# Optimization experiments

Measured on AMD Instinct MI355X. Metric: run time of the kernel, lower is better.

## Reference

```python
import jax, jax.numpy as jnp
import numpy as np

P = 50          # num_predicates
E = 2000        # num_entities
M = 64          # max_facts_per_query
F = 2_000_000   # num facts
N = 500_000     # num queries
BASE = E + 2    # pack base = max(constant_no, padding_idx) + 2


def setup_inputs() -> dict:
    key = jax.random.key(0)
    k1, k2, k3, k4, k5, k6 = jax.random.split(key, 6)
    fp = jax.random.randint(k1, (F,), 0, P, dtype=jnp.int32)
    fs = jax.random.randint(k2, (F,), 0, E, dtype=jnp.int32)
    fo = jax.random.randint(k3, (F,), 0, E, dtype=jnp.int32)
    facts_idx = jnp.stack([fp, fs, fo], axis=1)  # [F, 3]
    preds = jax.random.randint(k4, (N,), 0, P, dtype=jnp.int32)
    bound_args = jax.random.randint(k5, (N,), 0, E, dtype=jnp.int32)
    direction = jax.random.randint(k6, (N,), 0, 2, dtype=jnp.int32)
    return {"facts_idx": facts_idx, "preds": preds,
            "bound_args": bound_args, "direction": direction}


def _build_csr(keys, vals, num_buckets):
    """Sort vals by key; build offset table via scatter-add + cumsum (as in torch)."""
    order = jnp.argsort(keys)               # stable sort, matches pre-hash-sorted facts
    sorted_vals = vals[order]
    counts = jnp.zeros(num_buckets + 1, dtype=jnp.int32).at[keys + 1].add(1)
    offsets = jnp.cumsum(counts)
    return sorted_vals, offsets


def reference(facts_idx, preds, bound_args, direction):
    # --- _FactIndexBase: sort facts by packed 64-bit hash (lexicographic p,s,o) ---
    fp, fs, fo = facts_idx[:, 0], facts_idx[:, 1], facts_idx[:, 2]
    hashes = (fp * BASE + fs) * BASE + fo   # fits int32 for these dims
    h_order = jnp.argsort(hashes)
    fp, fs, fo = fp[h_order], fs[h_order], fo[h_order]

    # --- _build_inverted_indices: (pred,subj)->objs and (pred,obj)->subjs CSR ---
    ps_sorted_objs, ps_offsets = _build_csr(fp * E + fs, fo, P * E)
    po_sorted_subjs, po_offsets = _build_csr(fp * E + fo, fs, P * E)

    # --- enumerate() ---
    keys = preds * E + bound_args                               # [N]
    starts_ps = ps_offsets[keys]
    counts_ps = jnp.clip(ps_offsets[keys + 1] - starts_ps, 0, M)
    starts_po = po_offsets[keys]
    counts_po = jnp.clip(po_offsets[keys + 1] - starts_po, 0, M)
    is_obj = direction == 0                                     # [N] bool
    starts = jnp.where(is_obj, starts_ps, starts_po)
    counts = jnp.where(is_obj, counts_ps, counts_po)

    pos = jnp.arange(M, dtype=jnp.int32)[None, :]               # [1, M]
    valid = pos < counts[:, None]                               # [N, M]
    size = ps_sorted_objs.shape[0]                              # == F for both arrays
    gi = jnp.clip(starts[:, None] + pos, 0, size - 1)           # [N, M]
    vals_obj = ps_sorted_objs[gi]
    vals_subj = po_sorted_subjs[gi]
    candidates = jnp.where(is_obj[:, None], vals_obj, vals_subj)
    return candidates, valid
```

## Files before the change

### kernel.cpp

```cpp
#include <hip/hip_runtime.h>

#define PCONST 50
#define ECONST 2000
#define MCONST 64
#define NKEY   (PCONST * ECONST)
#define KPB    256
#define NBIN   ((NKEY + KPB - 1) / KPB)
#define NBIN2  (2 * NBIN)
#define SC_THREADS 1024
#define SC_CHUNK   8192
#define FPT    (SC_CHUNK / SC_THREADS)
#define CAP    6144

typedef int ivec4 __attribute__((ext_vector_type(4)));

__global__ void __launch_bounds__(SC_THREADS)
scatter_sort(const int* __restrict__ facts,
             int* __restrict__ bincur,
             unsigned* __restrict__ slab, int F) {
    __shared__ unsigned ordered[2 * SC_CHUNK];
    __shared__ int cnt[NBIN2];
    __shared__ int lbase[NBIN2];
    __shared__ int cur[NBIN2];
    __shared__ int base[NBIN2];
    __shared__ int wsum[16];

    int t = threadIdx.x;
    int blockStart = blockIdx.x * SC_CHUNK;
    int n = min(SC_CHUNK, F - blockStart);
    if (n <= 0) return;

    for (int i = t; i < NBIN2; i += SC_THREADS) cnt[i] = 0;
    __syncthreads();

    int myBase = blockStart + t * FPT;
    int myN = F - myBase;
    myN = (myN < 0) ? 0 : ((myN > FPT) ? FPT : myN);

    unsigned vps[FPT], vpo[FPT];

    if (myN == FPT) {
        const int4* p = (const int4*)(facts + 3 * myBase);
        int4 w0 = p[0], w1 = p[1], w2 = p[2], w3 = p[3], w4 = p[4], w5 = p[5];
        int kps, kpo;
        kps = w0.x * ECONST + w0.y; kpo = w0.x * ECONST + w0.z;
        vps[0] = ((unsigned)kps << 11) | (unsigned)w0.z;
        vpo[0] = ((unsigned)kpo << 11) | (unsigned)w0.y;
        atomicAdd(&cnt[kps >> 8], 1); atomicAdd(&cnt[NBIN + (kpo >> 8)], 1);
        kps = w0.w * ECONST + w1.x; kpo = w0.w * ECONST + w1.y;
        vps[1] = ((unsigned)kps << 11) | (unsigned)w1.y;
        vpo[1] = ((unsigned)kpo << 11) | (unsigned)w1.x;
        atomicAdd(&cnt[kps >> 8], 1); atomicAdd(&cnt[NBIN + (kpo >> 8)], 1);
        kps = w1.z * ECONST + w1.w; kpo = w1.z * ECONST + w2.x;
        vps[2] = ((unsigned)kps << 11) | (unsigned)w2.x;
        vpo[2] = ((unsigned)kpo << 11) | (unsigned)w1.w;
        atomicAdd(&cnt[kps >> 8], 1); atomicAdd(&cnt[NBIN + (kpo >> 8)], 1);
        kps = w2.y * ECONST + w2.z; kpo = w2.y * ECONST + w2.w;
        vps[3] = ((unsigned)kps << 11) | (unsigned)w2.w;
        vpo[3] = ((unsigned)kpo << 11) | (unsigned)w2.z;
        atomicAdd(&cnt[kps >> 8], 1); atomicAdd(&cnt[NBIN + (kpo >> 8)], 1);
        kps = w3.x * ECONST + w3.y; kpo = w3.x * ECONST + w3.z;
        vps[4] = ((unsigned)kps << 11) | (unsigned)w3.z;
        vpo[4] = ((unsigned)kpo << 11) | (unsigned)w3.y;
        atomicAdd(&cnt[kps >> 8], 1); atomicAdd(&cnt[NBIN + (kpo >> 8)], 1);
        kps = w3.w * ECONST + w4.x; kpo = w3.w * ECONST + w4.y;
        vps[5] = ((unsigned)kps << 11) | (unsigned)w4.y;
        vpo[5] = ((unsigned)kpo << 11) | (unsigned)w4.x;
        atomicAdd(&cnt[kps >> 8], 1); atomicAdd(&cnt[NBIN + (kpo >> 8)], 1);
        kps = w4.z * ECONST + w4.w; kpo = w4.z * ECONST + w5.x;
        vps[6] = ((unsigned)kps << 11) | (unsigned)w5.x;
        vpo[6] = ((unsigned)kpo << 11) | (unsigned)w4.w;
        atomicAdd(&cnt[kps >> 8], 1); atomicAdd(&cnt[NBIN + (kpo >> 8)], 1);
        kps = w5.y * ECONST + w5.z; kpo = w5.y * ECONST + w5.w;
        vps[7] = ((unsigned)kps << 11) | (unsigned)w5.w;
        vpo[7] = ((unsigned)kpo << 11) | (unsigned)w5.z;
        atomicAdd(&cnt[kps >> 8], 1); atomicAdd(&cnt[NBIN + (kpo >> 8)], 1);
    } else {
        for (int i = 0; i < myN; ++i) {
            int g = myBase + i;
            int fp = facts[3 * g], fs = facts[3 * g + 1], fo = facts[3 * g + 2];
            int kps = fp * ECONST + fs;
            int kpo = fp * ECONST + fo;
            vps[i] = ((unsigned)kps << 11) | (unsigned)fo;
            vpo[i] = ((unsigned)kpo << 11) | (unsigned)fs;
            atomicAdd(&cnt[kps >> 8], 1);
            atomicAdd(&cnt[NBIN + (kpo >> 8)], 1);
        }
    }
    __syncthreads();

    {
        int lane = t & 63, w = t >> 6;
        int c = (t < NBIN2) ? cnt[t] : 0;
        int inc = c;
        for (int d = 1; d < 64; d <<= 1) {
            int v = __shfl_up(inc, d);
            if (lane >= d) inc += v;
        }
        if (lane == 63) wsum[w] = inc;
        __syncthreads();
        if (t < NBIN2) {
            int wbase = 0;
            for (int i = 0; i < w; ++i) wbase += wsum[i];
            int excl = wbase + inc - c;
            lbase[t] = excl;
            cur[t]   = excl;
        }
    }
    __syncthreads();
    for (int i = t; i < NBIN2; i += SC_THREADS) {
        int c = cnt[i];
        base[i] = c ? atomicAdd(&bincur[i], c) : 0;
    }
    __syncthreads();

    #pragma unroll
    for (int i = 0; i < FPT; ++i) {
        if (i >= myN) break;
        unsigned ps = vps[i];
        int pos = atomicAdd(&cur[ps >> 19], 1);
        ordered[pos] = ps;
        unsigned po = vpo[i];
        pos = atomicAdd(&cur[NBIN + (po >> 19)], 1);
        ordered[pos] = (1u << 28) | po;
    }
    __syncthreads();

    int n2 = 2 * n;
    for (int j = t; j < n2; j += SC_THREADS) {
        unsigned v = ordered[j];
        int cbin = (int)((v >> 19) & 511u) + ((v >> 28) ? NBIN : 0);
        int pos  = base[cbin] + (j - lbase[cbin]);
        if (pos < CAP) slab[(size_t)cbin * CAP + pos] = v & 0x0FFFFFFFu;
    }
}

__global__ void binsort_kernel(const int* __restrict__ bincur,
                               const unsigned* __restrict__ slab,
                               unsigned* __restrict__ qtab,
                               unsigned short* __restrict__ dataA,
                               int F) {
    __shared__ unsigned short outv[CAP];
    __shared__ unsigned char  keyof[CAP];
    __shared__ int hist[KPB];
    __shared__ int sbase[KPB];
    __shared__ int wsum[4];
    __shared__ int red[4];

    int wg = blockIdx.x;
    int csr = (wg < NBIN) ? 0 : 1;
    int b   = wg - csr * NBIN;
    const int* curbase = bincur + csr * NBIN;
    int gofs = csr ? (F + 64) : 0;
    int t = threadIdx.x;
    int lane = t & 63, w = t >> 6;

    int s = 0;
    for (int i = t; i < b; i += KPB) s += curbase[i];
    for (int d = 1; d < 64; d <<= 1) s += __shfl_xor(s, d);
    if (lane == 0) red[w] = s;
    __syncthreads();
    int start = red[0] + red[1] + red[2] + red[3];

    int key0 = b * KPB;
    int len  = min(curbase[b], CAP);
    const unsigned* src = slab + (size_t)wg * CAP;

    hist[t] = 0;
    __syncthreads();

    for (int i = t; i < len; i += KPB)
        atomicAdd(&hist[(int)(src[i] >> 11) - key0], 1);
    __syncthreads();

    int c = hist[t];
    int inc = c;
    for (int d = 1; d < 64; d <<= 1) {
        int v = __shfl_up(inc, d);
        if (lane >= d) inc += v;
    }
    if (lane == 63) wsum[w] = inc;
    __syncthreads();
    int wbase = 0;
    for (int i = 0; i < w; ++i) wbase += wsum[i];
    int excl = wbase + inc - c;
    int gk = key0 + t;
    if (gk < NKEY)
        qtab[csr * NKEY + gk] =
            ((unsigned)(gofs + start + excl) << 7) | (unsigned)min(c, MCONST);
    sbase[t] = excl;
    hist[t]  = excl;
    __syncthreads();

    for (int i = t; i < len; i += KPB) {
        unsigned v = src[i];
        int lk  = (int)(v >> 11) - key0;
        int pos = atomicAdd(&hist[lk], 1);
        outv[pos]  = (unsigned short)(v & 2047u);
        keyof[pos] = (unsigned char)lk;
    }
    __syncthreads();

    for (int pos = t; pos < len; pos += KPB) {
        unsigned short v = outv[pos];
        int lk = (int)keyof[pos];
        int s0 = sbase[lk];
        int e0 = hist[lk];
        int rank = 0;
        for (int j = s0; j < e0; ++j) {
            unsigned short wv = outv[j];
            rank += (wv < v) || (wv == v && j < pos);
        }
        int gpos = start + s0 + rank;
        dataA[gofs + gpos] = v;
        if (gpos == F - 1) {
            for (int j = 0; j < 64; ++j) dataA[gofs + F + j] = v;
        }
    }
}

__global__ void query_kernel(const int* __restrict__ preds,
                             const int* __restrict__ bound,
                             const int* __restrict__ dir,
                             const unsigned* __restrict__ qtab,
                             const unsigned short* __restrict__ dataA,
                             int* __restrict__ cand,
                             int* __restrict__ valid, int N) {
    int gwave  = (blockIdx.x * blockDim.x + threadIdx.x) >> 6;
    int lane   = threadIdx.x & 63;
    int nwaves = (gridDim.x * blockDim.x) >> 6;
    int grp = lane >> 4;
    int sl  = (lane & 15) * 4;

    for (int qb = gwave * 64; qb < N; qb += nwaves * 64) {
        int q = qb + lane;
        unsigned pk = 0;
        if (q < N) {
            int idx = ((dir[q] != 0) ? NKEY : 0) + preds[q] * ECONST + bound[q];
            pk = qtab[idx];
        }
        int nq = min(64, N - qb);
        for (int j4 = 0; j4 < nq; j4 += 4) {
            int j = j4 + grp;
            unsigned pj = (unsigned)__shfl((int)pk, j);
            if (j < nq) {
                int c = (int)(pj & 127u);
                int s = (int)(pj >> 7);
                ivec4 cv, vv;
                cv.x = (int)dataA[s + sl];
                cv.y = (int)dataA[s + sl + 1];
                cv.z = (int)dataA[s + sl + 2];
                cv.w = (int)dataA[s + sl + 3];
                vv.x = (sl     < c) ? 1 : 0;
                vv.y = (sl + 1 < c) ? 1 : 0;
                vv.z = (sl + 2 < c) ? 1 : 0;
                vv.w = (sl + 3 < c) ? 1 : 0;
                size_t o = (size_t)(qb + j) * MCONST + sl;
                __builtin_nontemporal_store(cv, (ivec4*)&cand[o]);
                __builtin_nontemporal_store(vv, (ivec4*)&valid[o]);
            }
        }
    }
}

extern "C" void kernel_launch(void* const* d_in, const int* in_sizes, int n_in,
                              void* d_out, int out_size, void* d_ws, size_t ws_size,
                              hipStream_t stream) {
    const int* facts = (const int*)d_in[0];
    const int* preds = (const int*)d_in[1];
    const int* bound = (const int*)d_in[2];
    const int* dir   = (const int*)d_in[3];
    int F = in_sizes[0] / 3;
    int N = in_sizes[1];

    int* ws        = (int*)d_ws;
    unsigned* qtab = (unsigned*)ws;
    int* bincur    = ws + 2 * NKEY;
    int* pad       = bincur + NBIN2;
    size_t ofs = (size_t)(pad - ws);
    ofs = (ofs + 3) & ~(size_t)3;
    unsigned short* dataA = (unsigned short*)(ws + ofs);
    unsigned* slab = (unsigned*)(dataA + 2 * (size_t)F + 128);

    hipMemsetAsync(bincur, 0, (size_t)NBIN2 * sizeof(int), stream);

    int nChunks = (F + SC_CHUNK - 1) / SC_CHUNK;
    scatter_sort<<<nChunks, SC_THREADS, 0, stream>>>(facts, bincur, slab, F);
    binsort_kernel<<<NBIN2, KPB, 0, stream>>>(bincur, slab, qtab, dataA, F);

    int* cand  = (int*)d_out;
    int* valid = cand + (size_t)N * MCONST;
    int qBlocks = (N / 64 + 3) / 4 + 1;
    query_kernel<<<qBlocks, 256, 0, stream>>>(
        preds, bound, dir, qtab, dataA, cand, valid, N);
}
```

Measured before the change: 134.2 us.

## Fuse scatter, bin-sort and query kernels into one cooperative persistent kernel

Replaces the memset and three separate launches with a single cooperative kernel of 256 blocks of 1024 threads. Grid-wide syncs separate the phases: clearing the counters, per-chunk scatter into bins, per-bin sort (four 256-thread bin jobs per block, each with its own shared-memory segment) and the query gather. The aim is to remove launch gaps and the memset. In exchange the grid is fixed at one block per CU, which lowers occupancy in the bandwidth-bound query phase. The four bin jobs in a block also share block-wide barriers, so they wait on the slowest of the four.

Result: slower. 212.2 us (+58.2%).

```diff
diff --git a/kernel.cpp b/kernel.cpp
--- a/kernel.cpp
+++ b/kernel.cpp
@@ -1,4 +1,7 @@
 #include <hip/hip_runtime.h>
+#include <hip/hip_cooperative_groups.h>
+
+namespace cg = cooperative_groups;
 
 #define PCONST 50
 #define ECONST 2000
@@ -7,257 +10,277 @@
 #define KPB    256
 #define NBIN   ((NKEY + KPB - 1) / KPB)
 #define NBIN2  (2 * NBIN)
-#define SC_THREADS 1024
+#define BLOCK_THREADS 1024
+#define GRID_BLOCKS   256
 #define SC_CHUNK   8192
-#define FPT    (SC_CHUNK / SC_THREADS)
+#define FPT    (SC_CHUNK / BLOCK_THREADS)
 #define CAP    6144
+#define SEGSZ  20512
 
 typedef int ivec4 __attribute__((ext_vector_type(4)));
 
-__global__ void __launch_bounds__(SC_THREADS)
-scatter_sort(const int* __restrict__ facts,
+__global__ void __launch_bounds__(BLOCK_THREADS)
+fused_kernel(const int* __restrict__ facts,
+             const int* __restrict__ preds,
+             const int* __restrict__ bound,
+             const int* __restrict__ dir,
              int* __restrict__ bincur,
-             unsigned* __restrict__ slab, int F) {
-    __shared__ unsigned ordered[2 * SC_CHUNK];
-    __shared__ int cnt[NBIN2];
-    __shared__ int lbase[NBIN2];
-    __shared__ int cur[NBIN2];
-    __shared__ int base[NBIN2];
-    __shared__ int wsum[16];
-
-    int t = threadIdx.x;
-    int blockStart = blockIdx.x * SC_CHUNK;
-    int n = min(SC_CHUNK, F - blockStart);
-    if (n <= 0) return;
-
-    for (int i = t; i < NBIN2; i += SC_THREADS) cnt[i] = 0;
-    __syncthreads();
-
-    int myBase = blockStart + t * FPT;
-    int myN = F - myBase;
-    myN = (myN < 0) ? 0 : ((myN > FPT) ? FPT : myN);
-
-    unsigned vps[FPT], vpo[FPT];
-
-    if (myN == FPT) {
-        const int4* p = (const int4*)(facts + 3 * myBase);
-        int4 w0 = p[0], w1 = p[1], w2 = p[2], w3 = p[3], w4 = p[4], w5 = p[5];
-        int kps, kpo;
-        kps = w0.x * ECONST + w0.y; kpo = w0.x * ECONST + w0.z;
-        vps[0] = ((unsigned)kps << 11) | (unsigned)w0.z;
-        vpo[0] = ((unsigned)kpo << 11) | (unsigned)w0.y;
-        atomicAdd(&cnt[kps >> 8], 1); atomicAdd(&cnt[NBIN + (kpo >> 8)], 1);
-        kps = w0.w * ECONST + w1.x; kpo = w0.w * ECONST + w1.y;
-        vps[1] = ((unsigned)kps << 11) | (unsigned)w1.y;
-        vpo[1] = ((unsigned)kpo << 11) | (unsigned)w1.x;
-        atomicAdd(&cnt[kps >> 8], 1); atomicAdd(&cnt[NBIN + (kpo >> 8)], 1);
-        kps = w1.z * ECONST + w1.w; kpo = w1.z * ECONST + w2.x;
-        vps[2] = ((unsigned)kps << 11) | (unsigned)w2.x;
-        vpo[2] = ((unsigned)kpo << 11) | (unsigned)w1.w;
-        atomicAdd(&cnt[kps >> 8], 1); atomicAdd(&cnt[NBIN + (kpo >> 8)], 1);
-        kps = w2.y * ECONST + w2.z; kpo = w2.y * ECONST + w2.w;
-        vps[3] = ((unsigned)kps << 11) | (unsigned)w2.w;
-        vpo[3] = ((unsigned)kpo << 11) | (unsigned)w2.z;
-        atomicAdd(&cnt[kps >> 8], 1); atomicAdd(&cnt[NBIN + (kpo >> 8)], 1);
-        kps = w3.x * ECONST + w3.y; kpo = w3.x * ECONST + w3.z;
-        vps[4] = ((unsigned)kps << 11) | (unsigned)w3.z;
-        vpo[4] = ((unsigned)kpo << 11) | (unsigned)w3.y;
-        atomicAdd(&cnt[kps >> 8], 1); atomicAdd(&cnt[NBIN + (kpo >> 8)], 1);
-        kps = w3.w * ECONST + w4.x; kpo = w3.w * ECONST + w4.y;
-        vps[5] = ((unsigned)kps << 11) | (unsigned)w4.y;
-        vpo[5] = ((unsigned)kpo << 11) | (unsigned)w4.x;
-        atomicAdd(&cnt[kps >> 8], 1); atomicAdd(&cnt[NBIN + (kpo >> 8)], 1);
-        kps = w4.z * ECONST + w4.w; kpo = w4.z * ECONST + w5.x;
-        vps[6] = ((unsigned)kps << 11) | (unsigned)w5.x;
-        vpo[6] = ((unsigned)kpo << 11) | (unsigned)w4.w;
-        atomicAdd(&cnt[kps >> 8], 1); atomicAdd(&cnt[NBIN + (kpo >> 8)], 1);
-        kps = w5.y * ECONST + w5.z; kpo = w5.y * ECONST + w5.w;
-        vps[7] = ((unsigned)kps << 11) | (unsigned)w5.w;
-        vpo[7] = ((unsigned)kpo << 11) | (unsigned)w5.z;
-        atomicAdd(&cnt[kps >> 8], 1); atomicAdd(&cnt[NBIN + (kpo >> 8)], 1);
-    } else {
-        for (int i = 0; i < myN; ++i) {
-            int g = myBase + i;
-            int fp = facts[3 * g], fs = facts[3 * g + 1], fo = facts[3 * g + 2];
-            int kps = fp * ECONST + fs;
-            int kpo = fp * ECONST + fo;
-            vps[i] = ((unsigned)kps << 11) | (unsigned)fo;
-            vpo[i] = ((unsigned)kpo << 11) | (unsigned)fs;
-            atomicAdd(&cnt[kps >> 8], 1);
-            atomicAdd(&cnt[NBIN + (kpo >> 8)], 1);
+             unsigned* __restrict__ slab,
+             unsigned* __restrict__ qtab,
+             unsigned short* __restrict__ dataA,
+             int* __restrict__ cand,
+             int* __restrict__ valid,
+             int F, int N) {
+    cg::grid_group grid = cg::this_grid();
+    __shared__ __align__(16) unsigned char smem[4 * SEGSZ];
+
+    int t   = threadIdx.x;
+    int bid = blockIdx.x;
+
+    for (int i = bid * BLOCK_THREADS + t; i < NBIN2; i += GRID_BLOCKS * BLOCK_THREADS)
+        bincur[i] = 0;
+    grid.sync();
+
+    {
+        unsigned* ordered = (unsigned*)smem;
+        int* cnt   = (int*)(smem + 65536);
+        int* lbase = cnt + NBIN2;
+        int* cur   = lbase + NBIN2;
+        int* base  = cur + NBIN2;
+        int* wsum  = base + NBIN2;
+
+        int nChunks = (F + SC_CHUNK - 1) / SC_CHUNK;
+        for (int chunk = bid; chunk < nChunks; chunk += GRID_BLOCKS) {
+            int blockStart = chunk * SC_CHUNK;
+            int n = min(SC_CHUNK, F - blockStart);
+            if (n <= 0) break;
+
+            for (int i = t; i < NBIN2; i += BLOCK_THREADS) cnt[i] = 0;
+            __syncthreads();
+
+            int myBase = blockStart + t * FPT;
+            int myN = F - myBase;
+            myN = (myN < 0) ? 0 : ((myN > FPT) ? FPT : myN);
+
+            unsigned vps[FPT], vpo[FPT];
+
+            if (myN == FPT) {
+                const int4* p = (const int4*)(facts + 3 * myBase);
+                int4 w0 = p[0], w1 = p[1], w2 = p[2], w3 = p[3], w4 = p[4], w5 = p[5];
+                int kps, kpo;
+                kps = w0.x * ECONST + w0.y; kpo = w0.x * ECONST + w0.z;
+                vps[0] = ((unsigned)kps << 11) | (unsigned)w0.z;
+                vpo[0] = ((unsigned)kpo << 11) | (unsigned)w0.y;
+                atomicAdd(&cnt[kps >> 8], 1); atomicAdd(&cnt[NBIN + (kpo >> 8)], 1);
+                kps = w0.w * ECONST + w1.x; kpo = w0.w * ECONST + w1.y;
+                vps[1] = ((unsigned)kps << 11) | (unsigned)w1.y;
+                vpo[1] = ((unsigned)kpo << 11) | (unsigned)w1.x;
+                atomicAdd(&cnt[kps >> 8], 1); atomicAdd(&cnt[NBIN + (kpo >> 8)], 1);
+                kps = w1.z * ECONST + w1.w; kpo = w1.z * ECONST + w2.x;
+                vps[2] = ((unsigned)kps << 11) | (unsigned)w2.x;
+                vpo[2] = ((unsigned)kpo << 11) | (unsigned)w1.w;
+                atomicAdd(&cnt[kps >> 8], 1); atomicAdd(&cnt[NBIN + (kpo >> 8)], 1);
+                kps = w2.y * ECONST + w2.z; kpo = w2.y * ECONST + w2.w;
+                vps[3] = ((unsigned)kps << 11) | (unsigned)w2.w;
+                vpo[3] = ((unsigned)kpo << 11) | (unsigned)w2.z;
+                atomicAdd(&cnt[kps >> 8], 1); atomicAdd(&cnt[NBIN + (kpo >> 8)], 1);
+                kps = w3.x * ECONST + w3.y; kpo = w3.x * ECONST + w3.z;
+                vps[4] = ((unsigned)kps << 11) | (unsigned)w3.z;
+                vpo[4] = ((unsigned)kpo << 11) | (unsigned)w3.y;
+                atomicAdd(&cnt[kps >> 8], 1); atomicAdd(&cnt[NBIN + (kpo >> 8)], 1);
+                kps = w3.w * ECONST + w4.x; kpo = w3.w * ECONST + w4.y;
+                vps[5] = ((unsigned)kps << 11) | (unsigned)w4.y;
+                vpo[5] = ((unsigned)kpo << 11) | (unsigned)w4.x;
+                atomicAdd(&cnt[kps >> 8], 1); atomicAdd(&cnt[NBIN + (kpo >> 8)], 1);
+                kps = w4.z * ECONST + w4.w; kpo = w4.z * ECONST + w5.x;
+                vps[6] = ((unsigned)kps << 11) | (unsigned)w5.x;
+                vpo[6] = ((unsigned)kpo << 11) | (unsigned)w4.w;
+                atomicAdd(&cnt[kps >> 8], 1); atomicAdd(&cnt[NBIN + (kpo >> 8)], 1);
+                kps = w5.y * ECONST + w5.z; kpo = w5.y * ECONST + w5.w;
+                vps[7] = ((unsigned)kps << 11) | (unsigned)w5.w;
+                vpo[7] = ((unsigned)kpo << 11) | (unsigned)w5.z;
+                atomicAdd(&cnt[kps >> 8], 1); atomicAdd(&cnt[NBIN + (kpo >> 8)], 1);
+            } else {
+                for (int i = 0; i < myN; ++i) {
+                    int g = myBase + i;
+                    int fp = facts[3 * g], fs = facts[3 * g + 1], fo = facts[3 * g + 2];
+                    int kps = fp * ECONST + fs;
+                    int kpo = fp * ECONST + fo;
+                    vps[i] = ((unsigned)kps << 11) | (unsigned)fo;
+                    vpo[i] = ((unsigned)kpo << 11) | (unsigned)fs;
+                    atomicAdd(&cnt[kps >> 8], 1);
+                    atomicAdd(&cnt[NBIN + (kpo >> 8)], 1);
+                }
+            }
+            __syncthreads();
+
+            {
+                int lane = t & 63, w = t >> 6;
+                int c = (t < NBIN2) ? cnt[t] : 0;
+                int inc = c;
+                for (int d = 1; d < 64; d <<= 1) {
+                    int v = __shfl_up(inc, d);
+                    if (lane >= d) inc += v;
+                }
+                if (lane == 63) wsum[w] = inc;
+                __syncthreads();
+                if (t < NBIN2) {
+                    int wbase = 0;
+                    for (int i = 0; i < w; ++i) wbase += wsum[i];
+                    int excl = wbase + inc - c;
+                    lbase[t] = excl;
+                    cur[t]   = excl;
+                }
+            }
+            __syncthreads();
+            for (int i = t; i < NBIN2; i += BLOCK_THREADS) {
+                int c = cnt[i];
+                base[i] = c ? atomicAdd(&bincur[i], c) : 0;
+            }
+            __syncthreads();
+
+            #pragma unroll
+            for (int i = 0; i < FPT; ++i) {
+                if (i >= myN) break;
+                unsigned ps = vps[i];
+                int pos = atomicAdd(&cur[ps >> 19], 1);
+                ordered[pos] = ps;
+                unsigned po = vpo[i];
+                pos = atomicAdd(&cur[NBIN + (po >> 19)], 1);
+                ordered[pos] = (1u << 28) | po;
+            }
+            __syncthreads();
+
+            int n2 = 2 * n;
+            for (int j = t; j < n2; j += BLOCK_THREADS) {
+                unsigned v = ordered[j];
+                int cbin = (int)((v >> 19) & 511u) + ((v >> 28) ? NBIN : 0);
+                int pos  = base[cbin] + (j - lbase[cbin]);
+                if (pos < CAP) slab[(size_t)cbin * CAP + pos] = v & 0x0FFFFFFFu;
+            }
+            __syncthreads();
         }
     }
-    __syncthreads();
+    grid.sync();
 
     {
-        int lane = t & 63, w = t >> 6;
-        int c = (t < NBIN2) ? cnt[t] : 0;
+        int q  = t >> 8;
+        int tq = t & 255;
+        unsigned char* segp = smem + q * SEGSZ;
+        unsigned short* outv  = (unsigned short*)segp;
+        unsigned char*  keyof = segp + 2 * CAP;
+        int* hist  = (int*)(segp + 3 * CAP);
+        int* sbase = hist + KPB;
+        int* wsum4 = sbase + KPB;
+        int* red   = wsum4 + 4;
+
+        int wg  = bid * 4 + q;
+        bool vw = (wg < NBIN2);
+        int csr = (vw && wg < NBIN) ? 0 : 1;
+        int b   = vw ? (wg - csr * NBIN) : 0;
+        const int* curbase = bincur + csr * NBIN;
+        int gofs = csr ? (F + 64) : 0;
+        int lane = tq & 63, w = tq >> 6;
+
+        int s = 0;
+        for (int i = tq; i < b; i += KPB) s += curbase[i];
+        for (int d = 1; d < 64; d <<= 1) s += __shfl_xor(s, d);
+        if (lane == 0) red[w] = s;
+        __syncthreads();
+        int start = red[0] + red[1] + red[2] + red[3];
+
+        int key0 = b * KPB;
+        int len  = vw ? min(curbase[b], CAP) : 0;
+        const unsigned* src = slab + (size_t)(vw ? wg : 0) * CAP;
+
+        hist[tq] = 0;
+        __syncthreads();
+
+        for (int i = tq; i < len; i += KPB)
+            atomicAdd(&hist[(int)(src[i] >> 11) - key0], 1);
+        __syncthreads();
+
+        int c = hist[tq];
         int inc = c;
         for (int d = 1; d < 64; d <<= 1) {
             int v = __shfl_up(inc, d);
             if (lane >= d) inc += v;
         }
-        if (lane == 63) wsum[w] = inc;
-        __syncthreads();
-        if (t < NBIN2) {
-            int wbase = 0;
-            for (int i = 0; i < w; ++i) wbase += wsum[i];
-            int excl = wbase + inc - c;
-            lbase[t] = excl;
-            cur[t]   = excl;
+        if (lane == 63) wsum4[w] = inc;
+        __syncthreads();
+        int wbase = 0;
+        for (int i = 0; i < w; ++i) wbase += wsum4[i];
+        int excl = wbase + inc - c;
+        int gk = key0 + tq;
+        if (vw && gk < NKEY)
+            qtab[csr * NKEY + gk] =
+                ((unsigned)(gofs + start + excl) << 7) | (unsigned)min(c, MCONST);
+        sbase[tq] = excl;
+        hist[tq]  = excl;
+        __syncthreads();
+
+        for (int i = tq; i < len; i += KPB) {
+            unsigned v = src[i];
+            int lk  = (int)(v >> 11) - key0;
+            int pos = atomicAdd(&hist[lk], 1);
+            outv[pos]  = (unsigned short)(v & 2047u);
+            keyof[pos] = (unsigned char)lk;
+        }
+        __syncthreads();
+
+        for (int pos = tq; pos < len; pos += KPB) {
+            unsigned short v = outv[pos];
+            int lk = (int)keyof[pos];
+            int s0 = sbase[lk];
+            int e0 = hist[lk];
+            int rank = 0;
+            for (int j = s0; j < e0; ++j) {
+                unsigned short wv = outv[j];
+                rank += (wv < v) || (wv == v && j < pos);
+            }
+            int gpos = start + s0 + rank;
+            dataA[gofs + gpos] = v;
+            if (gpos == F - 1) {
+                for (int j = 0; j < 64; ++j) dataA[gofs + F + j] = v;
+            }
         }
     }
-    __syncthreads();
-    for (int i = t; i < NBIN2; i += SC_THREADS) {
-        int c = cnt[i];
-        base[i] = c ? atomicAdd(&bincur[i], c) : 0;
-    }
-    __syncthreads();
-
-    #pragma unroll
-    for (int i = 0; i < FPT; ++i) {
-        if (i >= myN) break;
-        unsigned ps = vps[i];
-        int pos = atomicAdd(&cur[ps >> 19], 1);
-        ordered[pos] = ps;
-        unsigned po = vpo[i];
-        pos = atomicAdd(&cur[NBIN + (po >> 19)], 1);
-        ordered[pos] = (1u << 28) | po;
-    }
-    __syncthreads();
-
-    int n2 = 2 * n;
-    for (int j = t; j < n2; j += SC_THREADS) {
-        unsigned v = ordered[j];
-        int cbin = (int)((v >> 19) & 511u) + ((v >> 28) ? NBIN : 0);
-        int pos  = base[cbin] + (j - lbase[cbin]);
-        if (pos < CAP) slab[(size_t)cbin * CAP + pos] = v & 0x0FFFFFFFu;
-    }
-}
-
-__global__ void binsort_kernel(const int* __restrict__ bincur,
-                               const unsigned* __restrict__ slab,
-                               unsigned* __restrict__ qtab,
-                               unsigned short* __restrict__ dataA,
-                               int F) {
-    __shared__ unsigned short outv[CAP];
-    __shared__ unsigned char  keyof[CAP];
-    __shared__ int hist[KPB];
-    __shared__ int sbase[KPB];
-    __shared__ int wsum[4];
-    __shared__ int red[4];
-
-    int wg = blockIdx.x;
-    int csr = (wg < NBIN) ? 0 : 1;
-    int b   = wg - csr * NBIN;
-    const int* curbase = bincur + csr * NBIN;
-    int gofs = csr ? (F + 64) : 0;
-    int t = threadIdx.x;
-    int lane = t & 63, w = t >> 6;
-
-    int s = 0;
-    for (int i = t; i < b; i += KPB) s += curbase[i];
-    for (int d = 1; d < 64; d <<= 1) s += __shfl_xor(s, d);
-    if (lane == 0) red[w] = s;
-    __syncthreads();
-    int start = red[0] + red[1] + red[2] + red[3];
-
-    int key0 = b * KPB;
-    int len  = min(curbase[b], CAP);
-    const unsigned* src = slab + (size_t)wg * CAP;
-
-    hist[t] = 0;
-    __syncthreads();
-
-    for (int i = t; i < len; i += KPB)
-        atomicAdd(&hist[(int)(src[i] >> 11) - key0], 1);
-    __syncthreads();
-
-    int c = hist[t];
-    int inc = c;
-    for (int d = 1; d < 64; d <<= 1) {
-        int v = __shfl_up(inc, d);
-        if (lane >= d) inc += v;
-    }
-    if (lane == 63) wsum[w] = inc;
-    __syncthreads();
-    int wbase = 0;
-    for (int i = 0; i < w; ++i) wbase += wsum[i];
-    int excl = wbase + inc - c;
-    int gk = key0 + t;
-    if (gk < NKEY)
-        qtab[csr * NKEY + gk] =
-            ((unsigned)(gofs + start + excl) << 7) | (unsigned)min(c, MCONST);
-    sbase[t] = excl;
-    hist[t]  = excl;
-    __syncthreads();
-
-    for (int i = t; i < len; i += KPB) {
-        unsigned v = src[i];
-        int lk  = (int)(v >> 11) - key0;
-        int pos = atomicAdd(&hist[lk], 1);
-        outv[pos]  = (unsigned short)(v & 2047u);
-        keyof[pos] = (unsigned char)lk;
-    }
-    __syncthreads();
-
-    for (int pos = t; pos < len; pos += KPB) {
-        unsigned short v = outv[pos];
-        int lk = (int)keyof[pos];
-        int s0 = sbase[lk];
-        int e0 = hist[lk];
-        int rank = 0;
-        for (int j = s0; j < e0; ++j) {
-            unsigned short wv = outv[j];
-            rank += (wv < v) || (wv == v && j < pos);
-        }
-        int gpos = start + s0 + rank;
-        dataA[gofs + gpos] = v;
-        if (gpos == F - 1) {
-            for (int j = 0; j < 64; ++j) dataA[gofs + F + j] = v;
-        }
-    }
-}
-
-__global__ void query_kernel(const int* __restrict__ preds,
-                             const int* __restrict__ bound,
-                             const int* __restrict__ dir,
-                             const unsigned* __restrict__ qtab,
-                             const unsigned short* __restrict__ dataA,
-                             int* __restrict__ cand,
-                             int* __restrict__ valid, int N) {
-    int gwave  = (blockIdx.x * blockDim.x + threadIdx.x) >> 6;
-    int lane   = threadIdx.x & 63;
-    int nwaves = (gridDim.x * blockDim.x) >> 6;
-    int grp = lane >> 4;
-    int sl  = (lane & 15) * 4;
-
-    for (int qb = gwave * 64; qb < N; qb += nwaves * 64) {
-        int q = qb + lane;
-        unsigned pk = 0;
-        if (q < N) {
-            int idx = ((dir[q] != 0) ? NKEY : 0) + preds[q] * ECONST + bound[q];
-            pk = qtab[idx];
-        }
-        int nq = min(64, N - qb);
-        for (int j4 = 0; j4 < nq; j4 += 4) {
-            int j = j4 + grp;
-            unsigned pj = (unsigned)__shfl((int)pk, j);
-            if (j < nq) {
-                int c = (int)(pj & 127u);
-                int s = (int)(pj >> 7);
-                ivec4 cv, vv;
-                cv.x = (int)dataA[s + sl];
-                cv.y = (int)dataA[s + sl + 1];
-                cv.z = (int)dataA[s + sl + 2];
-                cv.w = (int)dataA[s + sl + 3];
-                vv.x = (sl     < c) ? 1 : 0;
-                vv.y = (sl + 1 < c) ? 1 : 0;
-                vv.z = (sl + 2 < c) ? 1 : 0;
-                vv.w = (sl + 3 < c) ? 1 : 0;
-                size_t o = (size_t)(qb + j) * MCONST + sl;
-                __builtin_nontemporal_store(cv, (ivec4*)&cand[o]);
-                __builtin_nontemporal_store(vv, (ivec4*)&valid[o]);
+    grid.sync();
+
+    {
+        int gwave  = (bid * BLOCK_THREADS + t) >> 6;
+        int lane   = t & 63;
+        int nwaves = (GRID_BLOCKS * BLOCK_THREADS) >> 6;
+        int grp = lane >> 4;
+        int sl  = (lane & 15) * 4;
+
+        for (int qb = gwave * 64; qb < N; qb += nwaves * 64) {
+            int q = qb + lane;
+            unsigned pk = 0;
+            if (q < N) {
+                int idx = ((dir[q] != 0) ? NKEY : 0) + preds[q] * ECONST + bound[q];
+                pk = qtab[idx];
+            }
+            int nq = min(64, N - qb);
+            for (int j4 = 0; j4 < nq; j4 += 4) {
+                int j = j4 + grp;
+                unsigned pj = (unsigned)__shfl((int)pk, j);
+                if (j < nq) {
+                    int c = (int)(pj & 127u);
+                    int s = (int)(pj >> 7);
+                    ivec4 cv, vv;
+                    cv.x = (int)dataA[s + sl];
+                    cv.y = (int)dataA[s + sl + 1];
+                    cv.z = (int)dataA[s + sl + 2];
+                    cv.w = (int)dataA[s + sl + 3];
+                    vv.x = (sl     < c) ? 1 : 0;
+                    vv.y = (sl + 1 < c) ? 1 : 0;
+                    vv.z = (sl + 2 < c) ? 1 : 0;
+                    vv.w = (sl + 3 < c) ? 1 : 0;
+                    size_t o = (size_t)(qb + j) * MCONST + sl;
+                    __builtin_nontemporal_store(cv, (ivec4*)&cand[o]);
+                    __builtin_nontemporal_store(vv, (ivec4*)&valid[o]);
+                }
             }
         }
     }
@@ -282,15 +305,15 @@
     unsigned short* dataA = (unsigned short*)(ws + ofs);
     unsigned* slab = (unsigned*)(dataA + 2 * (size_t)F + 128);
 
-    hipMemsetAsync(bincur, 0, (size_t)NBIN2 * sizeof(int), stream);
-
-    int nChunks = (F + SC_CHUNK - 1) / SC_CHUNK;
-    scatter_sort<<<nChunks, SC_THREADS, 0, stream>>>(facts, bincur, slab, F);
-    binsort_kernel<<<NBIN2, KPB, 0, stream>>>(bincur, slab, qtab, dataA, F);
-
     int* cand  = (int*)d_out;
     int* valid = cand + (size_t)N * MCONST;
-    int qBlocks = (N / 64 + 3) / 4 + 1;
-    query_kernel<<<qBlocks, 256, 0, stream>>>(
-        preds, bound, dir, qtab, dataA, cand, valid, N);
+
+    void* args[] = {
+        (void*)&facts, (void*)&preds, (void*)&bound, (void*)&dir,
+        (void*)&bincur, (void*)&slab, (void*)&qtab, (void*)&dataA,
+        (void*)&cand, (void*)&valid, (void*)&F, (void*)&N
+    };
+    hipLaunchCooperativeKernel((const void*)fused_kernel,
+                               dim3(GRID_BLOCKS), dim3(BLOCK_THREADS),
+                               args, 0, stream);
 }
```

## Split scatter_sort into per-CSR blocks via a second grid dimension

Applied to the files above, without the earlier changes.

The scatter kernel now runs a 2D grid where blockIdx.y selects the (pred,subj) or (pred,obj) index, so each block bins only one key set. This halves per-block LDS (ordered buffer and bin arrays) and register state, which can raise occupancy and doubles the number of blocks. The cost is that every fact triple is read from global memory twice, once per CSR, and block-level overheads such as the histogram scan are repeated.

Result: no change. 135.4 us (+0.9%).

```diff
diff --git a/kernel.cpp b/kernel.cpp
--- a/kernel.cpp
+++ b/kernel.cpp
@@ -18,80 +18,56 @@
 scatter_sort(const int* __restrict__ facts,
              int* __restrict__ bincur,
              unsigned* __restrict__ slab, int F) {
-    __shared__ unsigned ordered[2 * SC_CHUNK];
-    __shared__ int cnt[NBIN2];
-    __shared__ int lbase[NBIN2];
-    __shared__ int cur[NBIN2];
-    __shared__ int base[NBIN2];
+    __shared__ unsigned ordered[SC_CHUNK];
+    __shared__ int cnt[NBIN];
+    __shared__ int lbase[NBIN];
+    __shared__ int cur[NBIN];
+    __shared__ int base[NBIN];
     __shared__ int wsum[16];
 
-    int t = threadIdx.x;
+    int t   = threadIdx.x;
+    int csr = blockIdx.y;
     int blockStart = blockIdx.x * SC_CHUNK;
     int n = min(SC_CHUNK, F - blockStart);
     if (n <= 0) return;
 
-    for (int i = t; i < NBIN2; i += SC_THREADS) cnt[i] = 0;
+    for (int i = t; i < NBIN; i += SC_THREADS) cnt[i] = 0;
     __syncthreads();
 
     int myBase = blockStart + t * FPT;
     int myN = F - myBase;
     myN = (myN < 0) ? 0 : ((myN > FPT) ? FPT : myN);
 
-    unsigned vps[FPT], vpo[FPT];
+    unsigned vpk[FPT];
 
     if (myN == FPT) {
         const int4* p = (const int4*)(facts + 3 * myBase);
         int4 w0 = p[0], w1 = p[1], w2 = p[2], w3 = p[3], w4 = p[4], w5 = p[5];
-        int kps, kpo;
-        kps = w0.x * ECONST + w0.y; kpo = w0.x * ECONST + w0.z;
-        vps[0] = ((unsigned)kps << 11) | (unsigned)w0.z;
-        vpo[0] = ((unsigned)kpo << 11) | (unsigned)w0.y;
-        atomicAdd(&cnt[kps >> 8], 1); atomicAdd(&cnt[NBIN + (kpo >> 8)], 1);
-        kps = w0.w * ECONST + w1.x; kpo = w0.w * ECONST + w1.y;
-        vps[1] = ((unsigned)kps << 11) | (unsigned)w1.y;
-        vpo[1] = ((unsigned)kpo << 11) | (unsigned)w1.x;
-        atomicAdd(&cnt[kps >> 8], 1); atomicAdd(&cnt[NBIN + (kpo >> 8)], 1);
-        kps = w1.z * ECONST + w1.w; kpo = w1.z * ECONST + w2.x;
-        vps[2] = ((unsigned)kps << 11) | (unsigned)w2.x;
-        vpo[2] = ((unsigned)kpo << 11) | (unsigned)w1.w;
-        atomicAdd(&cnt[kps >> 8], 1); atomicAdd(&cnt[NBIN + (kpo >> 8)], 1);
-        kps = w2.y * ECONST + w2.z; kpo = w2.y * ECONST + w2.w;
-        vps[3] = ((unsigned)kps << 11) | (unsigned)w2.w;
-        vpo[3] = ((unsigned)kpo << 11) | (unsigned)w2.z;
-        atomicAdd(&cnt[kps >> 8], 1); atomicAdd(&cnt[NBIN + (kpo >> 8)], 1);
-        kps = w3.x * ECONST + w3.y; kpo = w3.x * ECONST + w3.z;
-        vps[4] = ((unsigned)kps << 11) | (unsigned)w3.z;
-        vpo[4] = ((unsigned)kpo << 11) | (unsigned)w3.y;
-        atomicAdd(&cnt[kps >> 8], 1); atomicAdd(&cnt[NBIN + (kpo >> 8)], 1);
-        kps = w3.w * ECONST + w4.x; kpo = w3.w * ECONST + w4.y;
-        vps[5] = ((unsigned)kps << 11) | (unsigned)w4.y;
-        vpo[5] = ((unsigned)kpo << 11) | (unsigned)w4.x;
-        atomicAdd(&cnt[kps >> 8], 1); atomicAdd(&cnt[NBIN + (kpo >> 8)], 1);
-        kps = w4.z * ECONST + w4.w; kpo = w4.z * ECONST + w5.x;
-        vps[6] = ((unsigned)kps << 11) | (unsigned)w5.x;
-        vpo[6] = ((unsigned)kpo << 11) | (unsigned)w4.w;
-        atomicAdd(&cnt[kps >> 8], 1); atomicAdd(&cnt[NBIN + (kpo >> 8)], 1);
-        kps = w5.y * ECONST + w5.z; kpo = w5.y * ECONST + w5.w;
-        vps[7] = ((unsigned)kps << 11) | (unsigned)w5.w;
-        vpo[7] = ((unsigned)kpo << 11) | (unsigned)w5.z;
-        atomicAdd(&cnt[kps >> 8], 1); atomicAdd(&cnt[NBIN + (kpo >> 8)], 1);
+        int fp[FPT] = { w0.x, w0.w, w1.z, w2.y, w3.x, w3.w, w4.z, w5.y };
+        int fs[FPT] = { w0.y, w1.x, w1.w, w2.z, w3.y, w4.x, w4.w, w5.z };
+        int fo[FPT] = { w0.z, w1.y, w2.x, w2.w, w3.z, w4.y, w5.x, w5.w };
+        #pragma unroll
+        for (int i = 0; i < FPT; ++i) {
+            int key = fp[i] * ECONST + (csr ? fo[i] : fs[i]);
+            int val = csr ? fs[i] : fo[i];
+            vpk[i] = ((unsigned)key << 11) | (unsigned)val;
+            atomicAdd(&cnt[key >> 8], 1);
+        }
     } else {
         for (int i = 0; i < myN; ++i) {
             int g = myBase + i;
             int fp = facts[3 * g], fs = facts[3 * g + 1], fo = facts[3 * g + 2];
-            int kps = fp * ECONST + fs;
-            int kpo = fp * ECONST + fo;
-            vps[i] = ((unsigned)kps << 11) | (unsigned)fo;
-            vpo[i] = ((unsigned)kpo << 11) | (unsigned)fs;
-            atomicAdd(&cnt[kps >> 8], 1);
-            atomicAdd(&cnt[NBIN + (kpo >> 8)], 1);
+            int key = fp * ECONST + (csr ? fo : fs);
+            int val = csr ? fs : fo;
+            vpk[i] = ((unsigned)key << 11) | (unsigned)val;
+            atomicAdd(&cnt[key >> 8], 1);
         }
     }
     __syncthreads();
 
     {
         int lane = t & 63, w = t >> 6;
-        int c = (t < NBIN2) ? cnt[t] : 0;
+        int c = (t < NBIN) ? cnt[t] : 0;
         int inc = c;
         for (int d = 1; d < 64; d <<= 1) {
             int v = __shfl_up(inc, d);
@@ -99,39 +75,32 @@
         }
         if (lane == 63) wsum[w] = inc;
         __syncthreads();
-        if (t < NBIN2) {
+        if (t < NBIN) {
             int wbase = 0;
             for (int i = 0; i < w; ++i) wbase += wsum[i];
             int excl = wbase + inc - c;
             lbase[t] = excl;
             cur[t]   = excl;
-        }
-    }
-    __syncthreads();
-    for (int i = t; i < NBIN2; i += SC_THREADS) {
-        int c = cnt[i];
-        base[i] = c ? atomicAdd(&bincur[i], c) : 0;
+            int cc = c;
+            base[t] = cc ? atomicAdd(&bincur[csr * NBIN + t], cc) : 0;
+        }
     }
     __syncthreads();
 
     #pragma unroll
     for (int i = 0; i < FPT; ++i) {
         if (i >= myN) break;
-        unsigned ps = vps[i];
-        int pos = atomicAdd(&cur[ps >> 19], 1);
-        ordered[pos] = ps;
-        unsigned po = vpo[i];
-        pos = atomicAdd(&cur[NBIN + (po >> 19)], 1);
-        ordered[pos] = (1u << 28) | po;
-    }
-    __syncthreads();
-
-    int n2 = 2 * n;
-    for (int j = t; j < n2; j += SC_THREADS) {
+        unsigned v = vpk[i];
+        int pos = atomicAdd(&cur[v >> 19], 1);
+        ordered[pos] = v;
+    }
+    __syncthreads();
+
+    for (int j = t; j < n; j += SC_THREADS) {
         unsigned v = ordered[j];
-        int cbin = (int)((v >> 19) & 511u) + ((v >> 28) ? NBIN : 0);
-        int pos  = base[cbin] + (j - lbase[cbin]);
-        if (pos < CAP) slab[(size_t)cbin * CAP + pos] = v & 0x0FFFFFFFu;
+        int bin = (int)(v >> 19);
+        int pos = base[bin] + (j - lbase[bin]);
+        if (pos < CAP) slab[(size_t)(csr * NBIN + bin) * CAP + pos] = v;
     }
 }
 
@@ -285,7 +254,8 @@
     hipMemsetAsync(bincur, 0, (size_t)NBIN2 * sizeof(int), stream);
 
     int nChunks = (F + SC_CHUNK - 1) / SC_CHUNK;
-    scatter_sort<<<nChunks, SC_THREADS, 0, stream>>>(facts, bincur, slab, F);
+    dim3 sg(nChunks, 2);
+    scatter_sort<<<sg, SC_THREADS, 0, stream>>>(facts, bincur, slab, F);
     binsort_kernel<<<NBIN2, KPB, 0, stream>>>(bincur, slab, qtab, dataA, F);
 
     int* cand  = (int*)d_out;
```
